# Optimization experiments

Hardware: AMD Instinct MI355X
Metric: run time of the kernel (lower is better)

Reference implementation:

```python
import jax, jax.numpy as jnp
import numpy as np

EMB_DIM = 1024
NUM_HEADS = 16
SCALE_WEIGHTS = 1.0
TINY = jnp.finfo(jnp.float32).tiny


def setup_inputs() -> dict:
    key = jax.random.key(0)
    k1, k2, k3 = jax.random.split(key, 3)
    B, S = 2, 2048
    x = jax.random.normal(k1, (B, S, EMB_DIM), dtype=jnp.float32)
    weights = jax.random.uniform(k2, (B, S), dtype=jnp.float32)
    W_qkv = jax.random.normal(k3, (EMB_DIM, 3 * EMB_DIM), dtype=jnp.float32) / np.sqrt(EMB_DIM)
    b_qkv = jnp.zeros((3 * EMB_DIM,), dtype=jnp.float32)
    return {"x": x, "weights": weights, "W_qkv": W_qkv, "b_qkv": b_qkv}


def reference(x, weights, W_qkv, b_qkv):
    B, S, E = x.shape
    H = NUM_HEADS
    hd = E // H
    # QKV projection: [B,S,3E] -> [B,H,S,3*hd] -> split
    qkv = x @ W_qkv + b_qkv
    qkv = qkv.reshape(B, S, H, 3 * hd).transpose(0, 2, 1, 3)
    q, k, v = jnp.split(qkv, 3, axis=-1)  # each [B,H,S,hd]
    # weights: [B,S] -> [B,1,1,S] (broadcast over heads and query positions)
    w = weights[:, None, None, :]
    # scores with log-weight bias and hard masks
    attn_logits = jnp.einsum("bhqd,bhkd->bhqk", q, k) / jnp.sqrt(jnp.asarray(hd, x.dtype))
    attn_logits = attn_logits + jnp.log(w / SCALE_WEIGHTS + TINY)
    attn_logits = jnp.where(w == 0, -9e15, attn_logits)
    attn_logits = jnp.where(w == 1, 9e15, attn_logits)
    attention = jax.nn.softmax(attn_logits, axis=-1)
    values = jnp.einsum("bhqk,bhkd->bhqd", attention, v)
    return values.transpose(0, 2, 1, 3).reshape(B, S, E)
```

## Files before the change

### kernel.cpp

```cpp
#include <hip/hip_runtime.h>
#include <math.h>

#define B_  2
#define S_  2048
#define E_  1024
#define H_  16
#define HD_ 64
#define N3_ 3072
#define M_  (B_*S_)

typedef _Float16 h8  __attribute__((ext_vector_type(8)));
typedef _Float16 h4  __attribute__((ext_vector_type(4)));
typedef _Float16 h2  __attribute__((ext_vector_type(2)));
typedef __fp16   fp16x2 __attribute__((ext_vector_type(2)));
typedef float    f4  __attribute__((ext_vector_type(4)));
typedef float    fv16 __attribute__((ext_vector_type(16)));

typedef __attribute__((address_space(3))) unsigned int       lds_u32;
typedef const __attribute__((address_space(1))) unsigned int glob_u32;

__device__ __forceinline__ void gld16(const void* g, void* l) {
    __builtin_amdgcn_global_load_lds((glob_u32*)g, (lds_u32*)l, 16, 0, 0);
}
__device__ __forceinline__ float exp2_hw(float x) { return __builtin_amdgcn_exp2f(x); }
__device__ __forceinline__ float fmax3(float a, float b, float c) {
    return fmaxf(fmaxf(a, b), c);
}
__device__ __forceinline__ h2 cvt_pk_f16(float a, float b) {
    fp16x2 r = __builtin_amdgcn_cvt_pkrtz(a, b);
    return __builtin_bit_cast(h2, r);
}

#define QSCALE 0.18033688011112042f
#define RESCALE_THR 8.0f

__global__ __launch_bounds__(256) void prep_kernel(
        const float* __restrict__ x, _Float16* __restrict__ x16,
        const float* __restrict__ w, _Float16* __restrict__ w16,
        const float* __restrict__ W, _Float16* __restrict__ Wt) {
    __shared__ float T[64][65];
    int L = blockIdx.x;
    int tid = threadIdx.x;
    if (L < 2050) {
        const float* src = (L < 2048) ? &x[(size_t)L * 2048] : &w[(size_t)(L - 2048) * 2048];
        _Float16* dst    = (L < 2048) ? &x16[(size_t)L * 2048] : &w16[(size_t)(L - 2048) * 2048];
        int i = tid * 8;
        float4 u = *(const float4*)&src[i];
        float4 v = *(const float4*)&src[i + 4];
        h8 o;
        o[0] = (_Float16)u.x; o[1] = (_Float16)u.y; o[2] = (_Float16)u.z; o[3] = (_Float16)u.w;
        o[4] = (_Float16)v.x; o[5] = (_Float16)v.y; o[6] = (_Float16)v.z; o[7] = (_Float16)v.w;
        *(h8*)&dst[i] = o;
    } else {
        int L2 = L - 2050;
        int k0 = (L2 & 15) * 64, n0 = (L2 >> 4) * 64;
        int r = tid >> 4, c4 = (tid & 15) * 4;
#pragma unroll
        for (int i = 0; i < 4; i++) {
            int row = r + i * 16;
            float4 u = *(const float4*)&W[(size_t)(k0 + row) * N3_ + n0 + c4];
            T[c4 + 0][row] = u.x; T[c4 + 1][row] = u.y;
            T[c4 + 2][row] = u.z; T[c4 + 3][row] = u.w;
        }
        __syncthreads();
#pragma unroll
        for (int i = 0; i < 4; i++) {
            int rn = r + i * 16;
            h4 p;
            p[0] = (_Float16)T[rn][c4 + 0]; p[1] = (_Float16)T[rn][c4 + 1];
            p[2] = (_Float16)T[rn][c4 + 2]; p[3] = (_Float16)T[rn][c4 + 3];
            *(h4*)&Wt[(size_t)(n0 + rn) * E_ + k0 + c4] = p;
        }
    }
}

__global__ __launch_bounds__(256, 2) void qkv_gemm32(
        const _Float16* __restrict__ x16, const _Float16* __restrict__ wt,
        const float* __restrict__ bq, const float* __restrict__ w,
        _Float16* __restrict__ qws, _Float16* __restrict__ kws,
        _Float16* __restrict__ vtws) {
    __shared__ __align__(16) _Float16 Ab[2][128 * 64];
    __shared__ __align__(16) _Float16 Wb[2][192 * 64];

    int tid = threadIdx.x;
    int wid = tid >> 6, lane = tid & 63;
    int l31 = lane & 31, hi = lane >> 5, l7 = l31 & 7;
    int srow = lane >> 3;
    int wm = wid & 1, wn = wid >> 1;

    int L = blockIdx.x;
    int head = 2 * (L & 7) + (L >> 8);
    int mb = (L >> 3) & 31;
    int m0 = mb * 128;
    int n0 = head * 192;
    int b = m0 >> 11;
    int bh = b * H_ + head;
    int sblk = m0 & 2047;

    fv16 acc[2][3];
#pragma unroll
    for (int ntl = 0; ntl < 3; ntl++) {
        int n_abs = wn * 96 + ntl * 32;
        int which = n_abs >> 6;
        fv16 ini;
        if (which == 2) {
            float bb = bq[n0 + n_abs + l31];
#pragma unroll
            for (int r = 0; r < 16; r++) ini[r] = bb;
        } else {
#pragma unroll
            for (int g = 0; g < 4; g++) {
                f4 bv = *(const f4*)&bq[n0 + n_abs + 8 * g + 4 * hi];
#pragma unroll
                for (int j = 0; j < 4; j++) ini[4 * g + j] = bv[j];
            }
        }
        acc[0][ntl] = ini; acc[1][ntl] = ini;
    }

    auto stage = [&](int t, int bf) {
        int k0 = t * 64;
#pragma unroll
        for (int j = 0; j < 4; j++) {
            int batch = wid * 4 + j;
            int row = batch * 8 + srow;
            int ch = (lane & 7) ^ srow ^ (batch & 7);
            gld16(&x16[(size_t)(m0 + row) * E_ + k0 + ch * 8], &Ab[bf][batch * 8 * 64]);
        }
#pragma unroll
        for (int j = 0; j < 6; j++) {
            int batch = wid * 6 + j;
            int row = batch * 8 + srow;
            int ch = (lane & 7) ^ srow ^ (batch & 7);
            gld16(&wt[(size_t)(n0 + row) * E_ + k0 + ch * 8], &Wb[bf][batch * 8 * 64]);
        }
    };

    stage(0, 0);

    for (int t = 0; t < 16; t++) {
        int bf = t & 1;
        __syncthreads();
        if (t < 15) stage(t + 1, bf ^ 1);
#pragma unroll
        for (int step = 0; step < 4; step++) {
            h8 af[2], wf[3];
#pragma unroll
            for (int mt = 0; mt < 2; mt++) {
                int R = wm * 64 + mt * 32 + l31;
                int ph = ((2 * step + hi) ^ l7 ^ ((mt * 4 + (l31 >> 3)) & 7)) * 8;
                af[mt] = *(const h8*)&Ab[bf][R * 64 + ph];
            }
#pragma unroll
            for (int ntl = 0; ntl < 3; ntl++) {
                int R = wn * 96 + ntl * 32 + l31;
                int ph = ((2 * step + hi) ^ l7 ^ ((wn * 12 + ntl * 4 + (l31 >> 3)) & 7)) * 8;
                wf[ntl] = *(const h8*)&Wb[bf][R * 64 + ph];
            }
#pragma unroll
            for (int ntl = 0; ntl < 3; ntl++) {
                bool isv = (wn == 1) && (ntl >= 1);
#pragma unroll
                for (int mt = 0; mt < 2; mt++) {
                    if (isv)
                        acc[mt][ntl] = __builtin_amdgcn_mfma_f32_32x32x16_f16(af[mt], wf[ntl], acc[mt][ntl], 0, 0, 0);
                    else
                        acc[mt][ntl] = __builtin_amdgcn_mfma_f32_32x32x16_f16(wf[ntl], af[mt], acc[mt][ntl], 0, 0, 0);
                }
            }
        }
    }

#pragma unroll
    for (int ntl = 0; ntl < 3; ntl++) {
        int n_abs = wn * 96 + ntl * 32;
        int which = n_abs >> 6;
#pragma unroll
        for (int mt = 0; mt < 2; mt++) {
            if (which == 2) {
                int d = (n_abs & 63) + l31;
#pragma unroll
                for (int g = 0; g < 4; g++) {
                    int soff = wm * 64 + mt * 32 + 8 * g + 4 * hi;
                    f4 wf4 = *(const f4*)&w[m0 + soff];
                    h4 p;
#pragma unroll
                    for (int j = 0; j < 4; j++)
                        p[j] = (_Float16)(acc[mt][ntl][4 * g + j] * wf4[j]);
                    *(h4*)&vtws[((size_t)bh * 64 + d) * S_ + sblk + soff] = p;
                }
            } else {
                _Float16* dst = (which == 0) ? qws : kws;
                float scale = (which == 0) ? QSCALE : 1.0f;
                int s = sblk + wm * 64 + mt * 32 + l31;
#pragma unroll
                for (int g = 0; g < 4; g++) {
                    int d0 = (n_abs & 63) + 8 * g + 4 * hi;
                    h4 p;
#pragma unroll
                    for (int j = 0; j < 4; j++)
                        p[j] = (_Float16)(acc[mt][ntl][4 * g + j] * scale);
                    *(h4*)&dst[((size_t)bh * S_ + s) * 64 + d0] = p;
                }
            }
        }
    }
}

__global__ __launch_bounds__(256, 2) void attn_kernel(
        const _Float16* __restrict__ q, const _Float16* __restrict__ k,
        const _Float16* __restrict__ vt, const _Float16* __restrict__ w16,
        float* __restrict__ out) {
    __shared__ __align__(16) _Float16 Kb[2][64 * 64];
    __shared__ __align__(16) _Float16 Vb[3][64 * 64];
    __shared__ __align__(16) _Float16 lws16[2048];

    int tid = threadIdx.x;
    int wid = tid >> 6, lane = tid & 63;
    int l31 = lane & 31, hi = lane >> 5, l7 = l31 & 7;
    int srow = lane >> 3;
    int L = blockIdx.x;
    int bh = (L & 7) + 8 * (L >> 7);
    int qt = (L >> 3) & 15;
    int q0 = qt * 128;
    int b = bh >> 4, h = bh & 15;

    const _Float16* qbase = q + (size_t)bh * S_ * HD_;
    const _Float16* kbase = k + (size_t)bh * S_ * HD_;
    const _Float16* vbase = vt + (size_t)bh * HD_ * S_;
    const _Float16* wbase = w16 + (size_t)b * S_;

    gld16(&wbase[wid * 512 + lane * 8], &lws16[wid * 512]);

    auto vptr = [&](int i) -> _Float16* {
        return (i == 0) ? &Vb[0][0] : ((i == 1) ? &Vb[1][0] : &Vb[2][0]);
    };

    auto stage_kv = [&](int kt, _Float16* kdst, _Float16* vdst) {
        int k0 = kt * 64;
#pragma unroll
        for (int j = 0; j < 2; j++) {
            int batch = wid * 2 + j;
            int row = batch * 8 + srow;
            int ch = l7 ^ srow ^ (batch & 7);
            gld16(&kbase[(size_t)(k0 + row) * 64 + ch * 8], &kdst[batch * 8 * 64]);
            gld16(&vbase[(size_t)row * S_ + k0 + ch * 8], &vdst[batch * 8 * 64]);
        }
    };

    int qrow = q0 + wid * 32 + l31;
    h8 qf[4];
#pragma unroll
    for (int step = 0; step < 4; step++)
        qf[step] = *(const h8*)&qbase[(size_t)qrow * 64 + 16 * step + 8 * hi];

    fv16 o[2], ol;
    o[0] = (fv16)0.0f; o[1] = (fv16)0.0f; ol = (fv16)0.0f;
    float m_r = -INFINITY;

    auto qkt = [&](const _Float16* kbuf, fv16* stl) {
        stl[0] = (fv16)0.0f; stl[1] = (fv16)0.0f;
        __builtin_amdgcn_s_setprio(1);
#pragma unroll
        for (int step = 0; step < 4; step++)
#pragma unroll
            for (int kt2 = 0; kt2 < 2; kt2++) {
                int R = kt2 * 32 + l31;
                int ph = ((2 * step + hi) ^ l7 ^ ((kt2 * 4 + (l31 >> 3)) & 7)) * 8;
                h8 kf = *(const h8*)&kbuf[R * 64 + ph];
                stl[kt2] = __builtin_amdgcn_mfma_f32_32x32x16_f16(kf, qf[step], stl[kt2], 0, 0, 0);
            }
        __builtin_amdgcn_s_setprio(0);
    };

    auto softmax = [&](const fv16* stl, h4* pf) {
        float tm[11];
#pragma unroll
        for (int r = 0; r < 10; r++)
            tm[r] = fmax3(stl[(3*r)>>4][(3*r)&15], stl[(3*r+1)>>4][(3*r+1)&15],
                          stl[(3*r+2)>>4][(3*r+2)&15]);
        tm[10] = fmaxf(stl[1][14], stl[1][15]);
        float u0 = fmax3(tm[0], tm[1], tm[2]);
        float u1 = fmax3(tm[3], tm[4], tm[5]);
        float u2 = fmax3(tm[6], tm[7], tm[8]);
        float u3 = fmaxf(tm[9], tm[10]);
        float pmax = fmaxf(fmax3(u0, u1, u2), u3);

        if (!__all(pmax <= m_r + RESCALE_THR)) {
            float rowmax = fmaxf(pmax, __shfl_xor(pmax, 32));
            float mnew = fmaxf(m_r, rowmax);
            float alpha = exp2_hw(m_r - mnew);
            m_r = mnew;
            o[0] = o[0] * alpha;
            o[1] = o[1] * alpha;
            ol = ol * alpha;
        }

#pragma unroll
        for (int kt2 = 0; kt2 < 2; kt2++)
#pragma unroll
            for (int g = 0; g < 4; g++) {
                float e0 = exp2_hw(stl[kt2][4 * g + 0] - m_r);
                float e1 = exp2_hw(stl[kt2][4 * g + 1] - m_r);
                float e2 = exp2_hw(stl[kt2][4 * g + 2] - m_r);
                float e3 = exp2_hw(stl[kt2][4 * g + 3] - m_r);
                h2 p01 = cvt_pk_f16(e0, e1);
                h2 p23 = cvt_pk_f16(e2, e3);
                h4 p;
                p[0] = p01[0]; p[1] = p01[1]; p[2] = p23[0]; p[3] = p23[1];
                pf[kt2 * 4 + g] = p;
            }
    };

    auto pv = [&](const _Float16* vbuf, const h4* pf, int k0w) {
        __builtin_amdgcn_s_setprio(1);
#pragma unroll
        for (int kt2 = 0; kt2 < 2; kt2++)
#pragma unroll
            for (int g = 0; g < 4; g++) {
                int c = 4 * kt2 + g;
#pragma unroll
                for (int dt = 0; dt < 2; dt++) {
                    int R = dt * 32 + l31;
                    int ph = (c ^ l7 ^ ((dt * 4 + (l31 >> 3)) & 7)) * 8 + hi * 4;
                    h4 vf = *(const h4*)&vbuf[R * 64 + ph];
                    o[dt] = __builtin_amdgcn_mfma_f32_32x32x8f16(vf, pf[c], o[dt], 0, 0, 0);
                }
                h4 wf_ = *(const h4*)&lws16[k0w + c * 8 + 4 * hi];
                ol = __builtin_amdgcn_mfma_f32_32x32x8f16(wf_, pf[c], ol, 0, 0, 0);
            }
        __builtin_amdgcn_s_setprio(0);
    };

    stage_kv(0, &Kb[0][0], &Vb[0][0]);
    __syncthreads();
    stage_kv(1, &Kb[1][0], &Vb[1][0]);

    fv16 st[2];
    h4 pfA[8], pfB[8];
    qkt(&Kb[0][0], st);
    softmax(st, pfA);

    int vc = 0;
    for (int t = 0; t < 16; t++) {
        {
            int kt = 2 * t;
            __syncthreads();
            int vs = vc + 2; if (vs >= 3) vs -= 3;
            if (kt < 30) stage_kv(kt + 2, &Kb[0][0], vptr(vs));
            if (kt < 31) qkt(&Kb[1][0], st);
            pv(vptr(vc), pfA, kt * 64);
            if (kt < 31) softmax(st, pfB);
            vc = (vc == 2) ? 0 : vc + 1;
        }
        {
            int kt = 2 * t + 1;
            __syncthreads();
            int vs = vc + 2; if (vs >= 3) vs -= 3;
            if (kt < 30) stage_kv(kt + 2, &Kb[1][0], vptr(vs));
            if (kt < 31) qkt(&Kb[0][0], st);
            pv(vptr(vc), pfB, kt * 64);
            if (kt < 31) softmax(st, pfA);
            vc = (vc == 2) ? 0 : vc + 1;
        }
    }

    float linv = 1.0f / ol[0];
    float* obase = &out[((size_t)(b * S_ + qrow)) * E_ + h * 64];
#pragma unroll
    for (int dt = 0; dt < 2; dt++)
#pragma unroll
        for (int g = 0; g < 4; g++) {
            int d0 = dt * 32 + 8 * g + 4 * hi;
            f4 ov;
#pragma unroll
            for (int j = 0; j < 4; j++) ov[j] = o[dt][4 * g + j] * linv;
            *(f4*)&obase[d0] = ov;
        }
}

extern "C" void kernel_launch(void* const* d_in, const int* in_sizes, int n_in,
                              void* d_out, int out_size, void* d_ws, size_t ws_size,
                              hipStream_t stream) {
    const float* x  = (const float*)d_in[0];
    const float* w  = (const float*)d_in[1];
    const float* Wq = (const float*)d_in[2];
    const float* bq = (const float*)d_in[3];
    float* out = (float*)d_out;

    char* p = (char*)d_ws;
    _Float16* x16 = (_Float16*)p;              p += (size_t)M_ * E_ * 2;
    _Float16* wt  = (_Float16*)p;              p += (size_t)E_ * N3_ * 2;
    _Float16* qb  = (_Float16*)p;              p += (size_t)M_ * E_ * 2;
    _Float16* kb  = (_Float16*)p;              p += (size_t)M_ * E_ * 2;
    _Float16* vtb = (_Float16*)p;              p += (size_t)M_ * HD_ * H_ * 2;
    _Float16* w16 = (_Float16*)p;

    prep_kernel<<<dim3(2050 + 768), dim3(256), 0, stream>>>(x, x16, w, w16, Wq, wt);
    qkv_gemm32<<<dim3(512), dim3(256), 0, stream>>>(x16, wt, bq, w, qb, kb, vtb);
    attn_kernel<<<dim3(512), dim3(256), 0, stream>>>(qb, kb, vtb, w16, out);
}
```

Before: 178.2 us.

## Split attention into two independent online-softmax streams and remap QKV GEMM block-to-XCD assignment

Result: slower. 208.4 us (+16.9%).

```diff
diff --git a/kernel.cpp b/kernel.cpp
--- a/kernel.cpp
+++ b/kernel.cpp
@@ -89,8 +89,10 @@
     int wm = wid & 1, wn = wid >> 1;
 
     int L = blockIdx.x;
-    int head = 2 * (L & 7) + (L >> 8);
-    int mb = (L >> 3) & 31;
+    int xcd = L & 7;
+    int idx = L >> 3;
+    int head = (xcd & 1) * 8 + (idx & 7);
+    int mb   = (xcd >> 1) * 8 + (idx >> 3);
     int m0 = mb * 128;
     int n0 = head * 192;
     int b = m0 >> 11;
@@ -211,8 +213,8 @@
         const _Float16* __restrict__ q, const _Float16* __restrict__ k,
         const _Float16* __restrict__ vt, const _Float16* __restrict__ w16,
         float* __restrict__ out) {
-    __shared__ __align__(16) _Float16 Kb[2][64 * 64];
-    __shared__ __align__(16) _Float16 Vb[3][64 * 64];
+    __shared__ __align__(16) _Float16 Kb[4][64 * 64];
+    __shared__ __align__(16) _Float16 Vb[4][64 * 64];
     __shared__ __align__(16) _Float16 lws16[2048];
 
     int tid = threadIdx.x;
@@ -232,21 +234,20 @@
 
     gld16(&wbase[wid * 512 + lane * 8], &lws16[wid * 512]);
 
-    auto vptr = [&](int i) -> _Float16* {
-        return (i == 0) ? &Vb[0][0] : ((i == 1) ? &Vb[1][0] : &Vb[2][0]);
-    };
-
-    auto stage_kv = [&](int kt, _Float16* kdst, _Float16* vdst) {
+    auto stage1 = [&](int kt, int bf) {
         int k0 = kt * 64;
 #pragma unroll
         for (int j = 0; j < 2; j++) {
             int batch = wid * 2 + j;
             int row = batch * 8 + srow;
             int ch = l7 ^ srow ^ (batch & 7);
-            gld16(&kbase[(size_t)(k0 + row) * 64 + ch * 8], &kdst[batch * 8 * 64]);
-            gld16(&vbase[(size_t)row * S_ + k0 + ch * 8], &vdst[batch * 8 * 64]);
-        }
-    };
+            gld16(&kbase[(size_t)(k0 + row) * 64 + ch * 8], &Kb[bf][batch * 8 * 64]);
+            gld16(&vbase[(size_t)row * S_ + k0 + ch * 8], &Vb[bf][batch * 8 * 64]);
+        }
+    };
+
+    stage1(0, 0);
+    stage1(1, 1);
 
     int qrow = q0 + wid * 32 + l31;
     h8 qf[4];
@@ -254,9 +255,10 @@
     for (int step = 0; step < 4; step++)
         qf[step] = *(const h8*)&qbase[(size_t)qrow * 64 + 16 * step + 8 * hi];
 
-    fv16 o[2], ol;
-    o[0] = (fv16)0.0f; o[1] = (fv16)0.0f; ol = (fv16)0.0f;
-    float m_r = -INFINITY;
+    fv16 oA[2], oB[2], olA, olB;
+    oA[0] = (fv16)0.0f; oA[1] = (fv16)0.0f; olA = (fv16)0.0f;
+    oB[0] = (fv16)0.0f; oB[1] = (fv16)0.0f; olB = (fv16)0.0f;
+    float mA = -INFINITY, mB = -INFINITY;
 
     auto qkt = [&](const _Float16* kbuf, fv16* stl) {
         stl[0] = (fv16)0.0f; stl[1] = (fv16)0.0f;
@@ -273,7 +275,7 @@
         __builtin_amdgcn_s_setprio(0);
     };
 
-    auto softmax = [&](const fv16* stl, h4* pf) {
+    auto smax = [&](const fv16* stl, float& m_r, fv16* o, fv16& ol) {
         float tm[11];
 #pragma unroll
         for (int r = 0; r < 10; r++)
@@ -285,7 +287,6 @@
         float u2 = fmax3(tm[6], tm[7], tm[8]);
         float u3 = fmaxf(tm[9], tm[10]);
         float pmax = fmaxf(fmax3(u0, u1, u2), u3);
-
         if (!__all(pmax <= m_r + RESCALE_THR)) {
             float rowmax = fmaxf(pmax, __shfl_xor(pmax, 32));
             float mnew = fmaxf(m_r, rowmax);
@@ -295,7 +296,9 @@
             o[1] = o[1] * alpha;
             ol = ol * alpha;
         }
-
+    };
+
+    auto expp = [&](const fv16* stl, float m_r, h4* pf) {
 #pragma unroll
         for (int kt2 = 0; kt2 < 2; kt2++)
 #pragma unroll
@@ -312,60 +315,49 @@
             }
     };
 
-    auto pv = [&](const _Float16* vbuf, const h4* pf, int k0w) {
+    auto pv = [&](const _Float16* vbuf, const h4* pf, int k0w, fv16* o, fv16& ol) {
         __builtin_amdgcn_s_setprio(1);
 #pragma unroll
-        for (int kt2 = 0; kt2 < 2; kt2++)
-#pragma unroll
-            for (int g = 0; g < 4; g++) {
-                int c = 4 * kt2 + g;
-#pragma unroll
-                for (int dt = 0; dt < 2; dt++) {
-                    int R = dt * 32 + l31;
-                    int ph = (c ^ l7 ^ ((dt * 4 + (l31 >> 3)) & 7)) * 8 + hi * 4;
-                    h4 vf = *(const h4*)&vbuf[R * 64 + ph];
-                    o[dt] = __builtin_amdgcn_mfma_f32_32x32x8f16(vf, pf[c], o[dt], 0, 0, 0);
-                }
-                h4 wf_ = *(const h4*)&lws16[k0w + c * 8 + 4 * hi];
-                ol = __builtin_amdgcn_mfma_f32_32x32x8f16(wf_, pf[c], ol, 0, 0, 0);
-            }
+        for (int c = 0; c < 8; c++) {
+#pragma unroll
+            for (int dt = 0; dt < 2; dt++) {
+                int R = dt * 32 + l31;
+                int ph = (c ^ l7 ^ ((dt * 4 + (l31 >> 3)) & 7)) * 8 + hi * 4;
+                h4 vf = *(const h4*)&vbuf[R * 64 + ph];
+                o[dt] = __builtin_amdgcn_mfma_f32_32x32x8f16(vf, pf[c], o[dt], 0, 0, 0);
+            }
+            h4 wf_ = *(const h4*)&lws16[k0w + c * 8 + 4 * hi];
+            ol = __builtin_amdgcn_mfma_f32_32x32x8f16(wf_, pf[c], ol, 0, 0, 0);
+        }
         __builtin_amdgcn_s_setprio(0);
     };
 
-    stage_kv(0, &Kb[0][0], &Vb[0][0]);
-    __syncthreads();
-    stage_kv(1, &Kb[1][0], &Vb[1][0]);
-
-    fv16 st[2];
-    h4 pfA[8], pfB[8];
-    qkt(&Kb[0][0], st);
-    softmax(st, pfA);
-
-    int vc = 0;
-    for (int t = 0; t < 16; t++) {
-        {
-            int kt = 2 * t;
-            __syncthreads();
-            int vs = vc + 2; if (vs >= 3) vs -= 3;
-            if (kt < 30) stage_kv(kt + 2, &Kb[0][0], vptr(vs));
-            if (kt < 31) qkt(&Kb[1][0], st);
-            pv(vptr(vc), pfA, kt * 64);
-            if (kt < 31) softmax(st, pfB);
-            vc = (vc == 2) ? 0 : vc + 1;
-        }
-        {
-            int kt = 2 * t + 1;
-            __syncthreads();
-            int vs = vc + 2; if (vs >= 3) vs -= 3;
-            if (kt < 30) stage_kv(kt + 2, &Kb[1][0], vptr(vs));
-            if (kt < 31) qkt(&Kb[0][0], st);
-            pv(vptr(vc), pfB, kt * 64);
-            if (kt < 31) softmax(st, pfA);
-            vc = (vc == 2) ? 0 : vc + 1;
-        }
-    }
-
-    float linv = 1.0f / ol[0];
+    for (int it = 0; it < 16; it++) {
+        int t0 = 2 * it;
+        int B0 = (it & 1) * 2, B1 = B0 + 1;
+        __syncthreads();
+        if (it < 15) {
+            stage1(t0 + 2, B0 ^ 2);
+            stage1(t0 + 3, B1 ^ 2);
+        }
+
+        fv16 stA[2], stB[2];
+        qkt(&Kb[B0][0], stA);
+        qkt(&Kb[B1][0], stB);
+
+        h4 pfA[8], pfB[8];
+        smax(stA, mA, oA, olA);
+        expp(stA, mA, pfA);
+        pv(&Vb[B0][0], pfA, t0 * 64, oA, olA);
+        smax(stB, mB, oB, olB);
+        expp(stB, mB, pfB);
+        pv(&Vb[B1][0], pfB, t0 * 64 + 64, oB, olB);
+    }
+
+    float mm = fmaxf(mA, mB);
+    float aA = exp2_hw(mA - mm), aB = exp2_hw(mB - mm);
+    float linv = 1.0f / (olA[0] * aA + olB[0] * aB);
+    aA *= linv; aB *= linv;
     float* obase = &out[((size_t)(b * S_ + qrow)) * E_ + h * 64];
 #pragma unroll
     for (int dt = 0; dt < 2; dt++)
@@ -374,7 +366,8 @@
             int d0 = dt * 32 + 8 * g + 4 * hi;
             f4 ov;
 #pragma unroll
-            for (int j = 0; j < 4; j++) ov[j] = o[dt][4 * g + j] * linv;
+            for (int j = 0; j < 4; j++)
+                ov[j] = oA[dt][4 * g + j] * aA + oB[dt][4 * g + j] * aB;
             *(f4*)&obase[d0] = ov;
         }
 }
```
